# Kernel tuning notes

Hardware: AMD Instinct MI355X
Metric: run time of the kernel (lower is better)

The kernel has to match this reference:

```python
import jax, jax.numpy as jnp
import numpy as np

HEAD, DIM_IN, HDIM = 8, 256, 64
B, N = 4, 2048


def setup_inputs() -> dict:
    key = jax.random.key(0)
    k1, k2, k3, k4 = jax.random.split(key, 4)
    # xavier_uniform gain=1.414 bounds
    def xavier(k, shape, fan_in, fan_out):
        bound = 1.414 * np.sqrt(6.0 / (fan_in + fan_out))
        return jax.random.uniform(k, shape, jnp.float32, -bound, bound)
    h = jax.random.normal(k1, (B, N, DIM_IN), jnp.float32)
    w = xavier(k2, (HEAD, DIM_IN, HDIM), DIM_IN, HDIM)
    a_src = xavier(k3, (HEAD, HDIM, 1), HDIM, 1)
    a_dst = xavier(k4, (HEAD, HDIM, 1), HDIM, 1)
    b = jnp.zeros((HDIM,), jnp.float32)
    return {"h": h, "w": w, "a_src": a_src, "a_dst": a_dst, "b": b}


def reference(h, w, a_src, a_dst, b):
    # h: [B,N,Din], w: [H,Din,O] -> h_: [B,H,N,O]
    h_ = jnp.einsum("bnd,hdo->bhno", h, w)
    # additive attention logits per node: [B,H,N]
    src = jnp.einsum("bhno,ho->bhn", h_, a_src[..., 0])
    dst = jnp.einsum("bhno,ho->bhn", h_, a_dst[..., 0])
    # attn[b,h,i,j] = leaky_relu(src[i] + dst[j]); softmax over j
    logits = jax.nn.leaky_relu(src[..., :, None] + dst[..., None, :], negative_slope=0.2)
    attn = jax.nn.softmax(logits, axis=-1)  # [B,H,N,N]
    h_out = jnp.einsum("bhij,bhjo->bhio", attn, h_)
    return h_out + b
```

## Files before the change

kernel.cpp:

```cpp
#include <hip/hip_runtime.h>
#include <cstdint>
#include <cstddef>


#define HEADS 8
#define DIN   256
#define HDIM  64
#define NN    2048

typedef __attribute__((ext_vector_type(8))) _Float16 f16x8;
typedef __attribute__((ext_vector_type(2))) _Float16 f16x2;
typedef __attribute__((ext_vector_type(2))) __fp16   fp16x2;
typedef __attribute__((ext_vector_type(4))) float f32x4;

union H8 { f16x8 v; f16x2 p[4]; unsigned u[4]; };
union F2U { f16x2 h; fp16x2 q; unsigned u; };

__device__ __forceinline__ f16x2 pkrtz(float a, float b) {
  F2U t; t.q = __builtin_amdgcn_cvt_pkrtz(a, b);
  return t.h;
}
__device__ __forceinline__ unsigned pkrtz_u(float a, float b) {
  F2U t; t.q = __builtin_amdgcn_cvt_pkrtz(a, b);
  return t.u;
}

__global__ __launch_bounds__(256) void gat_prep(const float* __restrict__ w,
                                                const float* __restrict__ h,
                                                _Float16* __restrict__ wt,
                                                _Float16* __restrict__ hc) {
  const int bid = blockIdx.x;
  if (bid < 512) {
    const int idx = bid * 256 + threadIdx.x;
    const int o  = idx & 63;
    const int k  = (idx >> 6) & 255;
    const int hd = idx >> 14;
    wt[(hd * HDIM + o) * DIN + k] = (_Float16)w[idx];
  } else {
    const int idx = (bid - 512) * 256 + threadIdx.x;
    const float* p = h + (size_t)idx * 8;
    float4 x0 = ((const float4*)p)[0];
    float4 x1 = ((const float4*)p)[1];
    H8 o;
    o.p[0] = pkrtz(x0.x, x0.y); o.p[1] = pkrtz(x0.z, x0.w);
    o.p[2] = pkrtz(x1.x, x1.y); o.p[3] = pkrtz(x1.z, x1.w);
    *(f16x8*)(hc + (size_t)idx * 8) = o.v;
  }
}

__global__ __launch_bounds__(256) void gat_proj(const _Float16* __restrict__ hc,
                                                const _Float16* __restrict__ wt,
                                                const float* __restrict__ a_src,
                                                const float* __restrict__ a_dst,
                                                _Float16* __restrict__ h_t,
                                                float* __restrict__ src_s,
                                                float* __restrict__ dst_s) {
  const int head = blockIdx.x;
  const int rt   = blockIdx.y;
  const int tid  = threadIdx.x;
  const int w    = tid >> 6;
  const int lane = tid & 63;
  const int l15  = lane & 15, lg = lane >> 4;

  const int rowg = rt * 128 + w * 32;
  const _Float16* hb = hc + (size_t)rowg * DIN;
  const _Float16* wb = wt + head * (HDIM * DIN);

  f32x4 acc[2][4] = {};
#pragma unroll
  for (int kk = 0; kk < 8; ++kk) {
    const int k0 = kk * 32 + lg * 8;
    f16x8 af[2];
#pragma unroll
    for (int m = 0; m < 2; ++m)
      af[m] = *(const f16x8*)(hb + (size_t)(m * 16 + l15) * DIN + k0);
    f16x8 bfr[4];
#pragma unroll
    for (int n = 0; n < 4; ++n)
      bfr[n] = *(const f16x8*)(wb + (size_t)(n * 16 + l15) * DIN + k0);
#pragma unroll
    for (int m = 0; m < 2; ++m)
#pragma unroll
      for (int n = 0; n < 4; ++n)
        acc[m][n] = __builtin_amdgcn_mfma_f32_16x16x32_f16(af[m], bfr[n], acc[m][n], 0, 0, 0);
  }

  const int b   = (rt * 128) >> 11;
  const int nl0 = ((rt * 128) & 2047) + w * 32;
  const int bh  = b * HEADS + head;
  _Float16* hb_t = h_t + (size_t)bh * (256 * 512);
#pragma unroll
  for (int m = 0; m < 2; ++m)
#pragma unroll
    for (int n = 0; n < 4; ++n) {
      uint2 pk;
      pk.x = pkrtz_u(acc[m][n][0], acc[m][n][1]);
      pk.y = pkrtz_u(acc[m][n][2], acc[m][n][3]);
      const int j0 = nl0 + m * 16 + lg * 4;
      const int o  = n * 16 + l15;
      *(uint2*)(hb_t + (size_t)(j0 >> 3) * 512 + o * 8 + (j0 & 7)) = pk;
    }

  const float LOG2E = 1.4426950408889634f;
  float as4[4], ad4[4];
#pragma unroll
  for (int n = 0; n < 4; ++n) {
    as4[n] = a_src[head * HDIM + n * 16 + l15];
    ad4[n] = a_dst[head * HDIM + n * 16 + l15];
  }
#pragma unroll
  for (int m = 0; m < 2; ++m)
#pragma unroll
    for (int reg = 0; reg < 4; ++reg) {
      float ps = 0.f, pd = 0.f;
#pragma unroll
      for (int n = 0; n < 4; ++n) {
        float c = acc[m][n][reg];
        ps = fmaf(c, as4[n], ps);
        pd = fmaf(c, ad4[n], pd);
      }
#pragma unroll
      for (int off = 1; off <= 8; off <<= 1) {
        ps += __shfl_xor(ps, off);
        pd += __shfl_xor(pd, off);
      }
      if (l15 == 0) {
        const int nl = nl0 + m * 16 + lg * 4 + reg;
        src_s[(size_t)bh * NN + nl] = ps * LOG2E;
        dst_s[(size_t)bh * NN + nl] = pd * LOG2E;
      }
    }
}

__global__ __launch_bounds__(256) void gat_flash(const float* __restrict__ src_s,
                                                 const float* __restrict__ dst_s,
                                                 const _Float16* __restrict__ h_t,
                                                 const float* __restrict__ bias,
                                                 float* __restrict__ out) {
  const int it  = blockIdx.x;
  const int bh  = blockIdx.y;
  const int tid = threadIdx.x;
  const int w   = tid >> 6;
  const int lane = tid & 63;
  const int l15 = lane & 15, lg = lane >> 4;

  __shared__ _Float16 Ef[NN];
  __shared__ _Float16 Ff[NN];
  __shared__ float red[4];

  const float* dstp = dst_s + (size_t)bh * NN;
  const _Float16* vpan = h_t + (size_t)bh * (256 * 512);
  const _Float16* fb = vpan + lg * 512 + l15 * 8;

  float d[8];
  {
    float4 q0 = *(const float4*)(dstp + tid * 8);
    float4 q1 = *(const float4*)(dstp + tid * 8 + 4);
    d[0]=q0.x; d[1]=q0.y; d[2]=q0.z; d[3]=q0.w;
    d[4]=q1.x; d[5]=q1.y; d[6]=q1.z; d[7]=q1.w;
  }
  float dm = fmaxf(fmaxf(fmaxf(d[0],d[1]),fmaxf(d[2],d[3])),
                   fmaxf(fmaxf(d[4],d[5]),fmaxf(d[6],d[7])));
#pragma unroll
  for (int off = 32; off >= 1; off >>= 1) dm = fmaxf(dm, __shfl_xor(dm, off));
  if (lane == 0) red[w] = dm;
  __syncthreads();
  dm = fmaxf(fmaxf(red[0], red[1]), fmaxf(red[2], red[3]));

  {
    H8 e8, f8;
#pragma unroll
    for (int k = 0; k < 4; ++k) {
      float a0 = d[2*k]   - dm;
      float a1 = d[2*k+1] - dm;
      e8.p[k] = pkrtz(__builtin_amdgcn_exp2f(a0), __builtin_amdgcn_exp2f(a1));
      f8.p[k] = pkrtz(__builtin_amdgcn_exp2f(0.2f * a0),
                      __builtin_amdgcn_exp2f(0.2f * a1));
    }
    *(f16x8*)(&Ef[tid * 8]) = e8.v;
    *(f16x8*)(&Ff[tid * 8]) = f8.v;
  }
  __syncthreads();

  const float* srcp = src_s + (size_t)bh * NN + it * 256 + w * 64;
  f16x2 u2[4], v2[4];
#pragma unroll
  for (int m = 0; m < 4; ++m) {
    float sv   = srcp[m * 16 + l15];
    float smax = sv + dm;
    float mi   = fmaxf(smax, 0.2f * smax);
    float u    = __builtin_amdgcn_exp2f(smax - mi);
    float v    = __builtin_amdgcn_exp2f(fmaf(0.2f, smax, -mi));
    u2[m] = pkrtz(u, u);
    v2[m] = pkrtz(v, v);
  }

  f32x4 acc[4][4] = {};
  f32x4 accs[4]   = {};
  H8 onesU; onesU.u[0] = onesU.u[1] = onesU.u[2] = onesU.u[3] = 0x3C003C00u;
  const f16x8 ones = onesU.v;

  f16x8 V00, V01, V02, V03, V10, V11, V12, V13;
  f16x8 V20, V21, V22, V23, V30, V31, V32, V33;

#define LOADV(s, jc) do {                                              \
    const _Float16* fp_ = fb + (size_t)(jc) * 2048;                    \
    V##s##0 = *(const f16x8*)(fp_);                                    \
    V##s##1 = *(const f16x8*)(fp_ + 128);                              \
    V##s##2 = *(const f16x8*)(fp_ + 256);                              \
    V##s##3 = *(const f16x8*)(fp_ + 384);                              \
  } while (0)

#define STEP(s, jc) do {                                               \
    H8 eu_, fu_;                                                       \
    eu_.v = *(const f16x8*)(&Ef[(jc) * 32 + lg * 8]);                  \
    fu_.v = *(const f16x8*)(&Ff[(jc) * 32 + lg * 8]);                  \
    _Pragma("unroll") for (int m = 0; m < 4; ++m) {                    \
      H8 af_;                                                          \
      af_.p[0] = __builtin_elementwise_max(u2[m] * eu_.p[0], v2[m] * fu_.p[0]); \
      af_.p[1] = __builtin_elementwise_max(u2[m] * eu_.p[1], v2[m] * fu_.p[1]); \
      af_.p[2] = __builtin_elementwise_max(u2[m] * eu_.p[2], v2[m] * fu_.p[2]); \
      af_.p[3] = __builtin_elementwise_max(u2[m] * eu_.p[3], v2[m] * fu_.p[3]); \
      acc[m][0] = __builtin_amdgcn_mfma_f32_16x16x32_f16(af_.v, V##s##0, acc[m][0], 0, 0, 0); \
      acc[m][1] = __builtin_amdgcn_mfma_f32_16x16x32_f16(af_.v, V##s##1, acc[m][1], 0, 0, 0); \
      acc[m][2] = __builtin_amdgcn_mfma_f32_16x16x32_f16(af_.v, V##s##2, acc[m][2], 0, 0, 0); \
      acc[m][3] = __builtin_amdgcn_mfma_f32_16x16x32_f16(af_.v, V##s##3, acc[m][3], 0, 0, 0); \
      accs[m]   = __builtin_amdgcn_mfma_f32_16x16x32_f16(af_.v, ones, accs[m], 0, 0, 0);      \
    }                                                                  \
  } while (0)

  LOADV(0, 0);
  LOADV(1, 1);
  LOADV(2, 2);
#pragma unroll 1
  for (int t = 0; t < 60; t += 4) {
    LOADV(3, t + 3); STEP(0, t);
    LOADV(0, t + 4); STEP(1, t + 1);
    LOADV(1, t + 5); STEP(2, t + 2);
    LOADV(2, t + 6); STEP(3, t + 3);
  }
  LOADV(3, 63);
  STEP(0, 60); STEP(1, 61); STEP(2, 62); STEP(3, 63);

#undef LOADV
#undef STEP

  float bb[4];
#pragma unroll
  for (int n = 0; n < 4; ++n) bb[n] = bias[n * 16 + l15];

  float* ob = out + ((size_t)bh * NN + it * 256 + w * 64) * HDIM;
#pragma unroll
  for (int m = 0; m < 4; ++m)
#pragma unroll
    for (int reg = 0; reg < 4; ++reg) {
      const float linv = 1.0f / accs[m][reg];
      const int r = m * 16 + lg * 4 + reg;
#pragma unroll
      for (int n = 0; n < 4; ++n)
        ob[(size_t)r * HDIM + n * 16 + l15] = fmaf(acc[m][n][reg], linv, bb[n]);
    }
}

extern "C" void kernel_launch(void* const* d_in, const int* in_sizes, int n_in,
                              void* d_out, int out_size, void* d_ws, size_t ws_size,
                              hipStream_t stream) {
  const float* h     = (const float*)d_in[0];
  const float* w     = (const float*)d_in[1];
  const float* a_src = (const float*)d_in[2];
  const float* a_dst = (const float*)d_in[3];
  const float* bias  = (const float*)d_in[4];
  float* out = (float*)d_out;

  char* ws = (char*)d_ws;
  _Float16* wt  = (_Float16*)ws;
  _Float16* h_t = (_Float16*)(ws + 262144);
  float* src_s = (float*)(ws + 262144 + 8388608);
  float* dst_s = (float*)(ws + 262144 + 8388608 + 262144);

  _Float16* hcv = (_Float16*)d_out;

  hipLaunchKernelGGL(gat_prep,  dim3(1536),   dim3(256), 0, stream, w, h, wt, hcv);
  hipLaunchKernelGGL(gat_proj,  dim3(8, 64),  dim3(256), 0, stream,
                     hcv, wt, a_src, a_dst, h_t, src_s, dst_s);
  hipLaunchKernelGGL(gat_flash, dim3(8, 32),  dim3(256), 0, stream,
                     src_s, dst_s, h_t, bias, out);
}
```

Measured before the change: 52.09 us.

## Split flash kernel key range across two waves with LDS reduction

The attention kernel moves from 256-thread blocks, each covering 256 query rows, to 128-thread blocks covering 64 query rows. The two waves split the 2048 keys in half and combine their partial outputs and row sums through shared memory. This raises the grid from 256 to 1024 blocks so more CUs stay busy and each wave's serial loop is half as long. The cost is that every block recomputes the full exp tables for dst, each V panel is read by four times as many blocks, and there is an extra LDS reduction step.

Measured after the change: 54.30 us. 4.2% more time.

```diff
diff --git a/kernel.cpp b/kernel.cpp
--- a/kernel.cpp
+++ b/kernel.cpp
@@ -132,7 +132,7 @@
     }
 }
 
-__global__ __launch_bounds__(256) void gat_flash(const float* __restrict__ src_s,
+__global__ __launch_bounds__(128) void gat_flash(const float* __restrict__ src_s,
                                                  const float* __restrict__ dst_s,
                                                  const _Float16* __restrict__ h_t,
                                                  const float* __restrict__ bias,
@@ -146,43 +146,55 @@
 
   __shared__ _Float16 Ef[NN];
   __shared__ _Float16 Ff[NN];
-  __shared__ float red[4];
+  __shared__ f32x4 Oc[4][4][64];
+  __shared__ f32x4 Sc[4][64];
+  __shared__ float red[2];
 
   const float* dstp = dst_s + (size_t)bh * NN;
   const _Float16* vpan = h_t + (size_t)bh * (256 * 512);
   const _Float16* fb = vpan + lg * 512 + l15 * 8;
 
-  float d[8];
+  float d[16];
   {
-    float4 q0 = *(const float4*)(dstp + tid * 8);
-    float4 q1 = *(const float4*)(dstp + tid * 8 + 4);
-    d[0]=q0.x; d[1]=q0.y; d[2]=q0.z; d[3]=q0.w;
-    d[4]=q1.x; d[5]=q1.y; d[6]=q1.z; d[7]=q1.w;
-  }
-  float dm = fmaxf(fmaxf(fmaxf(d[0],d[1]),fmaxf(d[2],d[3])),
-                   fmaxf(fmaxf(d[4],d[5]),fmaxf(d[6],d[7])));
+    float4 q0 = *(const float4*)(dstp + tid * 16);
+    float4 q1 = *(const float4*)(dstp + tid * 16 + 4);
+    float4 q2 = *(const float4*)(dstp + tid * 16 + 8);
+    float4 q3 = *(const float4*)(dstp + tid * 16 + 12);
+    d[0]=q0.x; d[1]=q0.y; d[2]=q0.z;  d[3]=q0.w;
+    d[4]=q1.x; d[5]=q1.y; d[6]=q1.z;  d[7]=q1.w;
+    d[8]=q2.x; d[9]=q2.y; d[10]=q2.z; d[11]=q2.w;
+    d[12]=q3.x; d[13]=q3.y; d[14]=q3.z; d[15]=q3.w;
+  }
+  float dm = d[0];
+#pragma unroll
+  for (int k = 1; k < 16; ++k) dm = fmaxf(dm, d[k]);
 #pragma unroll
   for (int off = 32; off >= 1; off >>= 1) dm = fmaxf(dm, __shfl_xor(dm, off));
   if (lane == 0) red[w] = dm;
   __syncthreads();
-  dm = fmaxf(fmaxf(red[0], red[1]), fmaxf(red[2], red[3]));
+  dm = fmaxf(red[0], red[1]);
 
   {
-    H8 e8, f8;
-#pragma unroll
-    for (int k = 0; k < 4; ++k) {
-      float a0 = d[2*k]   - dm;
-      float a1 = d[2*k+1] - dm;
-      e8.p[k] = pkrtz(__builtin_amdgcn_exp2f(a0), __builtin_amdgcn_exp2f(a1));
-      f8.p[k] = pkrtz(__builtin_amdgcn_exp2f(0.2f * a0),
-                      __builtin_amdgcn_exp2f(0.2f * a1));
-    }
-    *(f16x8*)(&Ef[tid * 8]) = e8.v;
-    *(f16x8*)(&Ff[tid * 8]) = f8.v;
+    H8 e8[2], f8[2];
+#pragma unroll
+    for (int half = 0; half < 2; ++half)
+#pragma unroll
+      for (int k = 0; k < 4; ++k) {
+        float a0 = d[half * 8 + 2 * k]     - dm;
+        float a1 = d[half * 8 + 2 * k + 1] - dm;
+        e8[half].p[k] = pkrtz(__builtin_amdgcn_exp2f(a0),
+                              __builtin_amdgcn_exp2f(a1));
+        f8[half].p[k] = pkrtz(__builtin_amdgcn_exp2f(0.2f * a0),
+                              __builtin_amdgcn_exp2f(0.2f * a1));
+      }
+    *(f16x8*)(&Ef[tid * 16])     = e8[0].v;
+    *(f16x8*)(&Ef[tid * 16 + 8]) = e8[1].v;
+    *(f16x8*)(&Ff[tid * 16])     = f8[0].v;
+    *(f16x8*)(&Ff[tid * 16 + 8]) = f8[1].v;
   }
   __syncthreads();
 
-  const float* srcp = src_s + (size_t)bh * NN + it * 256 + w * 64;
+  const float* srcp = src_s + (size_t)bh * NN + it * 64;
   f16x2 u2[4], v2[4];
 #pragma unroll
   for (int m = 0; m < 4; ++m) {
@@ -199,6 +211,8 @@
   f32x4 accs[4]   = {};
   H8 onesU; onesU.u[0] = onesU.u[1] = onesU.u[2] = onesU.u[3] = 0x3C003C00u;
   const f16x8 ones = onesU.v;
+
+  const int jb = w * 32;
 
   f16x8 V00, V01, V02, V03, V10, V11, V12, V13;
   f16x8 V20, V21, V22, V23, V30, V31, V32, V33;
@@ -229,37 +243,52 @@
     }                                                                  \
   } while (0)
 
-  LOADV(0, 0);
-  LOADV(1, 1);
-  LOADV(2, 2);
+  LOADV(0, jb + 0);
+  LOADV(1, jb + 1);
+  LOADV(2, jb + 2);
 #pragma unroll 1
-  for (int t = 0; t < 60; t += 4) {
-    LOADV(3, t + 3); STEP(0, t);
-    LOADV(0, t + 4); STEP(1, t + 1);
-    LOADV(1, t + 5); STEP(2, t + 2);
-    LOADV(2, t + 6); STEP(3, t + 3);
-  }
-  LOADV(3, 63);
-  STEP(0, 60); STEP(1, 61); STEP(2, 62); STEP(3, 63);
+  for (int t = 0; t < 28; t += 4) {
+    LOADV(3, jb + t + 3); STEP(0, jb + t);
+    LOADV(0, jb + t + 4); STEP(1, jb + t + 1);
+    LOADV(1, jb + t + 5); STEP(2, jb + t + 2);
+    LOADV(2, jb + t + 6); STEP(3, jb + t + 3);
+  }
+  LOADV(3, jb + 31);
+  STEP(0, jb + 28); STEP(1, jb + 29); STEP(2, jb + 30); STEP(3, jb + 31);
 
 #undef LOADV
 #undef STEP
 
-  float bb[4];
-#pragma unroll
-  for (int n = 0; n < 4; ++n) bb[n] = bias[n * 16 + l15];
-
-  float* ob = out + ((size_t)bh * NN + it * 256 + w * 64) * HDIM;
-#pragma unroll
-  for (int m = 0; m < 4; ++m)
-#pragma unroll
-    for (int reg = 0; reg < 4; ++reg) {
-      const float linv = 1.0f / accs[m][reg];
-      const int r = m * 16 + lg * 4 + reg;
-#pragma unroll
-      for (int n = 0; n < 4; ++n)
-        ob[(size_t)r * HDIM + n * 16 + l15] = fmaf(acc[m][n][reg], linv, bb[n]);
+  if (w == 1) {
+#pragma unroll
+    for (int m = 0; m < 4; ++m) {
+      Sc[m][lane] = accs[m];
+#pragma unroll
+      for (int n = 0; n < 4; ++n) Oc[m][n][lane] = acc[m][n];
     }
+  }
+  __syncthreads();
+  if (w == 0) {
+    float bb[4];
+#pragma unroll
+    for (int n = 0; n < 4; ++n) bb[n] = bias[n * 16 + l15];
+
+    float* ob = out + ((size_t)bh * NN + it * 64) * HDIM;
+#pragma unroll
+    for (int m = 0; m < 4; ++m) {
+      f32x4 st = accs[m] + Sc[m][lane];
+#pragma unroll
+      for (int reg = 0; reg < 4; ++reg) {
+        const float linv = 1.0f / st[reg];
+        const int r = m * 16 + lg * 4 + reg;
+#pragma unroll
+        for (int n = 0; n < 4; ++n) {
+          float o = acc[m][n][reg] + Oc[m][n][lane][reg];
+          ob[(size_t)r * HDIM + n * 16 + l15] = fmaf(o, linv, bb[n]);
+        }
+      }
+    }
+  }
 }
 
 extern "C" void kernel_launch(void* const* d_in, const int* in_sizes, int n_in,
@@ -283,6 +312,6 @@
   hipLaunchKernelGGL(gat_prep,  dim3(1536),   dim3(256), 0, stream, w, h, wt, hcv);
   hipLaunchKernelGGL(gat_proj,  dim3(8, 64),  dim3(256), 0, stream,
                      hcv, wt, a_src, a_dst, h_t, src_s, dst_s);
-  hipLaunchKernelGGL(gat_flash, dim3(8, 32),  dim3(256), 0, stream,
+  hipLaunchKernelGGL(gat_flash, dim3(32, 32), dim3(128), 0, stream,
                      src_s, dst_s, h_t, bias, out);
 }
```
